# Kernel tuning notes

Hardware: AMD Instinct MI355X
Metric: run time of the kernel (lower is better)

Reference implementation:

```python
import jax, jax.numpy as jnp
import numpy as np

N, IN, OUT, H = 8192, 128, 64, 4
NEG_SLOPE = 0.2   # GATConv leaky-relu slope
EPS = 1e-5        # BatchNorm1d eps
MASK_VAL = -1e9   # masked_fill value for non-edges (finite for grad safety)


def setup_inputs() -> dict:
    key = jax.random.key(0)
    ks = jax.random.split(key, 5)
    x = jax.random.normal(ks[0], (N, IN), jnp.float32)
    adj = jax.random.randint(ks[1], (N, N), 0, 2, jnp.int32)  # dense 0/1 adjacency
    W = jax.random.normal(ks[2], (H, IN, OUT), jnp.float32) * (1.0 / np.sqrt(IN))
    a_i = jax.random.normal(ks[3], (H, OUT), jnp.float32) * (1.0 / np.sqrt(OUT))
    a_j = jax.random.normal(ks[4], (H, OUT), jnp.float32) * (1.0 / np.sqrt(OUT))
    gamma = jnp.ones((H * OUT,), jnp.float32)   # BN weight
    beta = jnp.zeros((H * OUT,), jnp.float32)   # BN bias
    return {"x": x, "adj": adj, "W": W, "a_i": a_i, "a_j": a_j,
            "gamma": gamma, "beta": beta}


def reference(x, adj, W, a_i, a_j, gamma, beta):
    # --- GATConv (dense adjacency, multi-head, concat) ---
    h = jnp.einsum('ni,hio->hno', x, W)              # [H, N, OUT]
    ei = jnp.einsum('hno,ho->hn', h, a_i)            # [H, N] source scores
    ej = jnp.einsum('hno,ho->hn', h, a_j)            # [H, N] target scores
    coe = ei[:, :, None] + ej[:, None, :]            # [H, N, N]
    coe = jnp.where(coe >= 0, coe, NEG_SLOPE * coe)  # leaky_relu
    coe = jnp.where(adj[None, :, :] == 0, MASK_VAL, coe)
    att = jax.nn.softmax(coe, axis=-1)               # segment softmax over neighbors
    out = jnp.einsum('hnm,hmo->hno', att, h)         # weighted aggregation
    out = jnp.transpose(out, (1, 0, 2)).reshape(N, H * OUT)  # concat heads
    # --- BatchNorm1d (training-mode batch stats over nodes) ---
    mean = jnp.mean(out, axis=0)
    var = jnp.var(out, axis=0)
    out = (out - mean) * jax.lax.rsqrt(var + EPS) * gamma + beta
    # --- ReLU ---
    return jax.nn.relu(out)
```

## Files before the change

kernel.cpp:

```cpp
#include <hip/hip_runtime.h>
#include <hip/hip_bf16.h>

#define NN   8192
#define IND  128
#define OUTD 64
#define NH   4
#define NEG_SLOPE 0.2f
#define BN_EPS 1e-5f

typedef __attribute__((ext_vector_type(8))) short bf16x8;
typedef __attribute__((ext_vector_type(4))) float f32x4;
typedef __attribute__((ext_vector_type(4))) int   i32x4;

static __device__ __forceinline__ float bf2f(short s) {
    union { unsigned u; float f; } v; v.u = ((unsigned)(unsigned short)s) << 16; return v.f;
}
static __device__ __forceinline__ short f2bf(float f) {
    union { float f; unsigned u; } v; v.f = f;
    return (short)((v.u + 0x8000u) >> 16);
}

__global__ void GATModule_7636451852431_kernel(float* out) {
    out[0] = 1000.0f;
}

__global__ __launch_bounds__(256) void k0_repackW(const float* __restrict__ W,
                                                  short* __restrict__ WB) {
    int tid = blockIdx.x * 256 + threadIdx.x;
    int o = tid & 63, i = (tid >> 6) & 127, h = tid >> 13;
    WB[((h * 16 + (i >> 3)) * 64 + o) * 8 + (i & 7)] = f2bf(W[(h * 128 + i) * 64 + o]);
}

__global__ __launch_bounds__(256) void k1_feat(const float* __restrict__ x,
                                               const short* __restrict__ WB,
                                               const float* __restrict__ a_i,
                                               const float* __restrict__ a_j,
                                               short* __restrict__ hB,
                                               float* __restrict__ t_ei,  float* __restrict__ t_E1i,
                                               float* __restrict__ t_E2i, float* __restrict__ t_nj,
                                               float* __restrict__ t_E1j, float* __restrict__ t_E2j) {
    int w = threadIdx.x >> 6;
    int l = threadIdx.x & 63;
    int quad = l >> 4, lx = l & 15;
    int rb = blockIdx.x;

    f32x4 acc[4] = {};
#pragma unroll
    for (int ks = 0; ks < 4; ++ks) {
        const float* xp = x + (rb * 16 + lx) * IND + ks * 32 + quad * 8;
        f32x4 xa = *(const f32x4*)xp;
        f32x4 xb = *(const f32x4*)(xp + 4);
        bf16x8 af;
#pragma unroll
        for (int j = 0; j < 4; ++j) { af[j] = f2bf(xa[j]); af[4 + j] = f2bf(xb[j]); }
#pragma unroll
        for (int ot = 0; ot < 4; ++ot) {
            bf16x8 bf = *(const bf16x8*)(WB + ((w * 16 + ks * 4 + quad) * 64 + ot * 16 + lx) * 8);
            acc[ot] = __builtin_amdgcn_mfma_f32_16x16x32_bf16(af, bf, acc[ot], 0, 0, 0);
        }
    }
    float aiv[4], ajv[4];
#pragma unroll
    for (int ot = 0; ot < 4; ++ot) {
        aiv[ot] = a_i[w * 64 + ot * 16 + lx];
        ajv[ot] = a_j[w * 64 + ot * 16 + lx];
    }
#pragma unroll
    for (int reg = 0; reg < 4; ++reg) {
        int row = rb * 16 + quad * 4 + reg;
        float ei = 0.f, ej = 0.f;
#pragma unroll
        for (int ot = 0; ot < 4; ++ot) {
            float hv = acc[ot][reg];
            ei += hv * aiv[ot];
            ej += hv * ajv[ot];
        }
#pragma unroll
        for (int m = 1; m <= 8; m <<= 1) {
            ei += __shfl_xor(ei, m, 64);
            ej += __shfl_xor(ej, m, 64);
        }
        if (lx == reg) {
            t_ei [w * NN + row] = ei;
            t_E1i[w * NN + row] = expf(ei);
            t_E2i[w * NN + row] = expf(NEG_SLOPE * ei);
            t_nj [w * NN + row] = -ej;
            t_E1j[w * NN + row] = expf(ej);
            t_E2j[w * NN + row] = expf(NEG_SLOPE * ej);
        }
#pragma unroll
        for (int ot = 0; ot < 4; ++ot) {
            int o = ot * 16 + lx;
            hB[((w * 1024 + (row >> 3)) * 64 + o) * 8 + (row & 7)] = f2bf(acc[ot][reg]);
        }
    }
}

__global__ __launch_bounds__(256) void k2_attn(const int* __restrict__ adj,
                                               const short* __restrict__ hB,
                                               const float* __restrict__ t_ei,
                                               const float* __restrict__ t_E1i,
                                               const float* __restrict__ t_E2i,
                                               const float* __restrict__ t_nj,
                                               const float* __restrict__ t_E1j,
                                               const float* __restrict__ t_E2j,
                                               float* __restrict__ num,
                                               float* __restrict__ Lsum) {
    int w = threadIdx.x >> 6;
    int l = threadIdx.x & 63;
    int quad = l >> 4, lx = l & 15;
    int rb = blockIdx.x >> 2, ks = blockIdx.x & 3;
    int rowbase = rb * 64;
    int tb = w * NN;

    float eiv[4], E1i[4], E2i[4];
#pragma unroll
    for (int r = 0; r < 4; ++r) {
        int i = rowbase + r * 16 + lx;
        eiv[r] = t_ei[tb + i];
        E1i[r] = t_E1i[tb + i];
        E2i[r] = t_E2i[tb + i];
    }

    f32x4 acc[4][4] = {};
    float Lacc[4] = {0.f, 0.f, 0.f, 0.f};
    int k0 = ks * 2048;

#pragma unroll 1
    for (int kt = 0; kt < 64; ++kt) {
        int kb = k0 + kt * 32 + quad * 8;
        f32x4 nj0  = *(const f32x4*)(t_nj  + tb + kb);
        f32x4 nj1  = *(const f32x4*)(t_nj  + tb + kb + 4);
        f32x4 e1j0 = *(const f32x4*)(t_E1j + tb + kb);
        f32x4 e1j1 = *(const f32x4*)(t_E1j + tb + kb + 4);
        f32x4 e2j0 = *(const f32x4*)(t_E2j + tb + kb);
        f32x4 e2j1 = *(const f32x4*)(t_E2j + tb + kb + 4);

        bf16x8 bfrag[4];
#pragma unroll
        for (int ot = 0; ot < 4; ++ot)
            bfrag[ot] = *(const bf16x8*)(hB + ((w * 1024 + (kb >> 3)) * 64 + ot * 16 + lx) * 8);

        bf16x8 afr[4];
#pragma unroll
        for (int r = 0; r < 4; ++r) {
            const int* ap = adj + (size_t)(rowbase + r * 16 + lx) * NN + kb;
            i32x4 a0 = *(const i32x4*)ap;
            i32x4 a1 = *(const i32x4*)(ap + 4);
            bf16x8 af;
            float lsum = 0.f;
#pragma unroll
            for (int j = 0; j < 8; ++j) {
                int   av = (j < 4) ? a0[j] : a1[j - 4];
                float nj = (j < 4) ? nj0[j] : nj1[j - 4];
                float e1 = (j < 4) ? e1j0[j] : e1j1[j - 4];
                float e2 = (j < 4) ? e2j0[j] : e2j1[j - 4];
                bool  c  = eiv[r] >= nj;
                float p  = (c ? E1i[r] : E2i[r]) * (c ? e1 : e2);
                p = av ? p : 0.0f;
                short ps = f2bf(p);
                af[j] = ps;
                lsum += bf2f(ps);
            }
            Lacc[r] += lsum;
            afr[r] = af;
        }
#pragma unroll
        for (int r = 0; r < 4; ++r)
#pragma unroll
            for (int ot = 0; ot < 4; ++ot)
                acc[r][ot] = __builtin_amdgcn_mfma_f32_16x16x32_bf16(afr[r], bfrag[ot], acc[r][ot], 0, 0, 0);
    }

#pragma unroll
    for (int r = 0; r < 4; ++r) {
        float L = Lacc[r];
        L += __shfl_xor(L, 16, 64);
        L += __shfl_xor(L, 32, 64);
        if (l < 16)
            atomicAdd(&Lsum[w * NN + rowbase + r * 16 + lx], L);
    }
#pragma unroll
    for (int r = 0; r < 4; ++r)
#pragma unroll
        for (int ot = 0; ot < 4; ++ot)
#pragma unroll
            for (int reg = 0; reg < 4; ++reg) {
                int row = rowbase + r * 16 + quad * 4 + reg;
                atomicAdd(&num[row * 256 + w * 64 + ot * 16 + lx], acc[r][ot][reg]);
            }
}

__global__ __launch_bounds__(256) void k3_combine(float* __restrict__ num,
                                                  const float* __restrict__ Lsum,
                                                  float* __restrict__ stats) {
    int c = threadIdx.x;
    int h = c >> 6;
    float s = 0.f, s2 = 0.f;
    for (int rr = 0; rr < 32; ++rr) {
        int row = blockIdx.x * 32 + rr;
        float L = Lsum[h * NN + row];
        float val = num[row * 256 + c] / L;
        num[row * 256 + c] = val;
        s += val; s2 += val * val;
    }
    atomicAdd(&stats[c], s);
    atomicAdd(&stats[c + 256], s2);
}

__global__ __launch_bounds__(256) void k4_bnfinal(const float* __restrict__ stats,
                                                  const float* __restrict__ gamma,
                                                  const float* __restrict__ beta,
                                                  float* __restrict__ bnp) {
    int c = threadIdx.x;
    float mean = stats[c] * (1.0f / NN);
    float var  = stats[c + 256] * (1.0f / NN) - mean * mean;
    float sc = gamma[c] * rsqrtf(var + BN_EPS);
    bnp[c] = sc;
    bnp[c + 256] = beta[c] - mean * sc;
}

__global__ __launch_bounds__(256) void k5_apply(const float* __restrict__ preout,
                                                const float* __restrict__ bnp,
                                                const short* __restrict__ hB,
                                                const float* __restrict__ Lsum,
                                                float* __restrict__ out) {
    int g = blockIdx.x * 256 + threadIdx.x;
    f32x4 v = *(const f32x4*)(preout + (size_t)g * 4);
    int cb = (g * 4) & 255;
    f32x4 r;
#pragma unroll
    for (int j = 0; j < 4; ++j) {
        float y = v[j] * bnp[cb + j] + bnp[256 + cb + j];
        if (!(y == y)) y = 54321.0f;
        else y = fmaxf(y, 0.0f);
        r[j] = y;
    }
    if (g == 0) {
        float sh = 0.f;
        for (int j = 0; j < 8; ++j) sh += fabsf(bf2f(hB[j]));
        float sl = Lsum[0];
        float sp = 0.f;
        for (int rr = 0; rr < 4; ++rr) {
            const float* pr = preout + (size_t)(rr * 2111) * 256;
            for (int c = 0; c < 256; ++c) sp += fabsf(pr[c]);
        }
        float sentinel = 0.f;
        if (!(sh > 1e-6f))      sentinel = 30000.f;
        else if (!(sl > 1.0f))  sentinel = 40000.f;
        else if (!(sp > 1e-6f)) sentinel = 20000.f;
        else if (!(sp == sp))   sentinel = 50000.f;
        if (sentinel != 0.f) r[0] = sentinel;
    }
    *(f32x4*)(out + (size_t)g * 4) = r;
}

extern "C" void kernel_launch(void* const* d_in, const int* in_sizes, int n_in,
                              void* d_out, int out_size, void* d_ws, size_t ws_size,
                              hipStream_t stream) {
    (void)in_sizes; (void)n_in; (void)out_size; (void)ws_size;
    const float* x     = (const float*)d_in[0];
    const int*   adj   = (const int*)d_in[1];
    const float* W     = (const float*)d_in[2];
    const float* a_i   = (const float*)d_in[3];
    const float* a_j   = (const float*)d_in[4];
    const float* gamma = (const float*)d_in[5];
    const float* beta  = (const float*)d_in[6];
    float* out = (float*)d_out;

    char* ws = (char*)d_ws;
    short* WB    = (short*)(ws + 0);
    short* hB    = (short*)(ws + 65536);
    float* t_ei  = (float*)(ws + 4259840);
    float* t_E1i = t_ei + 32768;
    float* t_E2i = t_ei + 2 * 32768;
    float* t_nj  = t_ei + 3 * 32768;
    float* t_E1j = t_ei + 4 * 32768;
    float* t_E2j = t_ei + 5 * 32768;
    float* num   = (float*)(ws + 5046272);
    float* Lsum  = (float*)(ws + 13434880);
    float* stats = (float*)(ws + 13565952);
    float* bnp   = (float*)(ws + 13568000);

    hipMemsetAsync(num,   0, 8388608, stream);
    hipMemsetAsync(Lsum,  0, 131072, stream);
    hipMemsetAsync(stats, 0, 2048, stream);

    GATModule_7636451852431_kernel<<<dim3(1), dim3(1), 0, stream>>>(out);
    k0_repackW<<<dim3(128), dim3(256), 0, stream>>>(W, WB);
    k1_feat   <<<dim3(512), dim3(256), 0, stream>>>(x, WB, a_i, a_j, hB,
                                                    t_ei, t_E1i, t_E2i, t_nj, t_E1j, t_E2j);
    k2_attn   <<<dim3(512), dim3(256), 0, stream>>>(adj, hB, t_ei, t_E1i, t_E2i,
                                                    t_nj, t_E1j, t_E2j, num, Lsum);
    k3_combine<<<dim3(256), dim3(256), 0, stream>>>(num, Lsum, stats);
    k4_bnfinal<<<dim3(1),   dim3(256), 0, stream>>>(stats, gamma, beta, bnp);
    k5_apply  <<<dim3(2048), dim3(256), 0, stream>>>(num, bnp, hB, Lsum, out);
}
```

Baseline: 589.8 us.

## Split attention K range 8-way, pack bf16 via perm, drop debug sentinels

Doubles the split-K factor of the attention kernel, launching 1024 blocks with 1024 columns each and unrolling the loop by two, so more waves are available to hide adj loads. It also packs two bf16 values with a single perm instruction and sums the softmax denominator from the unrounded fp32 values. Separately, it merges the three memsets into one, removes the dummy kernel, and drops the debug sentinel checks from the apply kernel. The cost is more atomic traffic on num and Lsum, and a denominator that no longer exactly matches the bf16-rounded numerator weights.

Result: slower. 631.6 us (+7.1%).

```diff
diff --git a/kernel.cpp b/kernel.cpp
--- a/kernel.cpp
+++ b/kernel.cpp
@@ -18,10 +18,6 @@
 static __device__ __forceinline__ short f2bf(float f) {
     union { float f; unsigned u; } v; v.f = f;
     return (short)((v.u + 0x8000u) >> 16);
-}
-
-__global__ void GATModule_7636451852431_kernel(float* out) {
-    out[0] = 1000.0f;
 }
 
 __global__ __launch_bounds__(256) void k0_repackW(const float* __restrict__ W,
@@ -109,7 +105,7 @@
     int w = threadIdx.x >> 6;
     int l = threadIdx.x & 63;
     int quad = l >> 4, lx = l & 15;
-    int rb = blockIdx.x >> 2, ks = blockIdx.x & 3;
+    int rb = blockIdx.x >> 3, ks = blockIdx.x & 7;
     int rowbase = rb * 64;
     int tb = w * NN;
 
@@ -124,10 +120,10 @@
 
     f32x4 acc[4][4] = {};
     float Lacc[4] = {0.f, 0.f, 0.f, 0.f};
-    int k0 = ks * 2048;
-
-#pragma unroll 1
-    for (int kt = 0; kt < 64; ++kt) {
+    int k0 = ks * 1024;
+
+#pragma unroll 2
+    for (int kt = 0; kt < 32; ++kt) {
         int kb = k0 + kt * 32 + quad * 8;
         f32x4 nj0  = *(const f32x4*)(t_nj  + tb + kb);
         f32x4 nj1  = *(const f32x4*)(t_nj  + tb + kb + 4);
@@ -147,23 +143,32 @@
             const int* ap = adj + (size_t)(rowbase + r * 16 + lx) * NN + kb;
             i32x4 a0 = *(const i32x4*)ap;
             i32x4 a1 = *(const i32x4*)(ap + 4);
-            bf16x8 af;
+            union { i32x4 i; bf16x8 b; } af;
             float lsum = 0.f;
 #pragma unroll
-            for (int j = 0; j < 8; ++j) {
-                int   av = (j < 4) ? a0[j] : a1[j - 4];
-                float nj = (j < 4) ? nj0[j] : nj1[j - 4];
-                float e1 = (j < 4) ? e1j0[j] : e1j1[j - 4];
-                float e2 = (j < 4) ? e2j0[j] : e2j1[j - 4];
-                bool  c  = eiv[r] >= nj;
-                float p  = (c ? E1i[r] : E2i[r]) * (c ? e1 : e2);
-                p = av ? p : 0.0f;
-                short ps = f2bf(p);
-                af[j] = ps;
-                lsum += bf2f(ps);
+            for (int jj = 0; jj < 4; ++jj) {
+                int j0 = 2 * jj, j1 = 2 * jj + 1;
+                int   av0 = (j0 < 4) ? a0[j0] : a1[j0 - 4];
+                int   av1 = (j1 < 4) ? a0[j1] : a1[j1 - 4];
+                float njA = (j0 < 4) ? nj0[j0] : nj1[j0 - 4];
+                float njB = (j1 < 4) ? nj0[j1] : nj1[j1 - 4];
+                float e1A = (j0 < 4) ? e1j0[j0] : e1j1[j0 - 4];
+                float e1B = (j1 < 4) ? e1j0[j1] : e1j1[j1 - 4];
+                float e2A = (j0 < 4) ? e2j0[j0] : e2j1[j0 - 4];
+                float e2B = (j1 < 4) ? e2j0[j1] : e2j1[j1 - 4];
+                bool  cA  = eiv[r] >= njA;
+                bool  cB  = eiv[r] >= njB;
+                float p0  = (cA ? E1i[r] : E2i[r]) * (cA ? e1A : e2A);
+                float p1  = (cB ? E1i[r] : E2i[r]) * (cB ? e1B : e2B);
+                p0 = av0 ? p0 : 0.0f;
+                p1 = av1 ? p1 : 0.0f;
+                lsum += p0 + p1;
+                unsigned u0 = __float_as_uint(p0) + 0x8000u;
+                unsigned u1 = __float_as_uint(p1) + 0x8000u;
+                af.i[jj] = (int)__builtin_amdgcn_perm(u1, u0, 0x07060302);
             }
             Lacc[r] += lsum;
-            afr[r] = af;
+            afr[r] = af.b;
         }
 #pragma unroll
         for (int r = 0; r < 4; ++r)
@@ -222,36 +227,14 @@
 
 __global__ __launch_bounds__(256) void k5_apply(const float* __restrict__ preout,
                                                 const float* __restrict__ bnp,
-                                                const short* __restrict__ hB,
-                                                const float* __restrict__ Lsum,
                                                 float* __restrict__ out) {
     int g = blockIdx.x * 256 + threadIdx.x;
     f32x4 v = *(const f32x4*)(preout + (size_t)g * 4);
     int cb = (g * 4) & 255;
     f32x4 r;
 #pragma unroll
-    for (int j = 0; j < 4; ++j) {
-        float y = v[j] * bnp[cb + j] + bnp[256 + cb + j];
-        if (!(y == y)) y = 54321.0f;
-        else y = fmaxf(y, 0.0f);
-        r[j] = y;
-    }
-    if (g == 0) {
-        float sh = 0.f;
-        for (int j = 0; j < 8; ++j) sh += fabsf(bf2f(hB[j]));
-        float sl = Lsum[0];
-        float sp = 0.f;
-        for (int rr = 0; rr < 4; ++rr) {
-            const float* pr = preout + (size_t)(rr * 2111) * 256;
-            for (int c = 0; c < 256; ++c) sp += fabsf(pr[c]);
-        }
-        float sentinel = 0.f;
-        if (!(sh > 1e-6f))      sentinel = 30000.f;
-        else if (!(sl > 1.0f))  sentinel = 40000.f;
-        else if (!(sp > 1e-6f)) sentinel = 20000.f;
-        else if (!(sp == sp))   sentinel = 50000.f;
-        if (sentinel != 0.f) r[0] = sentinel;
-    }
+    for (int j = 0; j < 4; ++j)
+        r[j] = fmaxf(v[j] * bnp[cb + j] + bnp[256 + cb + j], 0.0f);
     *(f32x4*)(out + (size_t)g * 4) = r;
 }
 
@@ -282,17 +265,14 @@
     float* stats = (float*)(ws + 13565952);
     float* bnp   = (float*)(ws + 13568000);
 
-    hipMemsetAsync(num,   0, 8388608, stream);
-    hipMemsetAsync(Lsum,  0, 131072, stream);
-    hipMemsetAsync(stats, 0, 2048, stream);
-
-    GATModule_7636451852431_kernel<<<dim3(1), dim3(1), 0, stream>>>(out);
+    hipMemsetAsync(num, 0, 8388608 + 131072 + 2048, stream);
+
     k0_repackW<<<dim3(128), dim3(256), 0, stream>>>(W, WB);
     k1_feat   <<<dim3(512), dim3(256), 0, stream>>>(x, WB, a_i, a_j, hB,
                                                     t_ei, t_E1i, t_E2i, t_nj, t_E1j, t_E2j);
-    k2_attn   <<<dim3(512), dim3(256), 0, stream>>>(adj, hB, t_ei, t_E1i, t_E2i,
-                                                    t_nj, t_E1j, t_E2j, num, Lsum);
+    k2_attn   <<<dim3(1024), dim3(256), 0, stream>>>(adj, hB, t_ei, t_E1i, t_E2i,
+                                                     t_nj, t_E1j, t_E2j, num, Lsum);
     k3_combine<<<dim3(256), dim3(256), 0, stream>>>(num, Lsum, stats);
     k4_bnfinal<<<dim3(1),   dim3(256), 0, stream>>>(stats, gamma, beta, bnp);
-    k5_apply  <<<dim3(2048), dim3(256), 0, stream>>>(num, bnp, hB, Lsum, out);
-}
+    k5_apply  <<<dim3(2048), dim3(256), 0, stream>>>(num, bnp, out);
+}
```
